# Optimization experiments

Measured on AMD Instinct MI355X. Metric: run time of the kernel, lower is better.

## Reference

```python
import jax, jax.numpy as jnp
import numpy as np
from jax.scipy.special import gammaln, logsumexp

N_SAMPLE, N_GENE, N_TYPE, N_BATCH = 50000, 128, 16, 4


def setup_inputs() -> dict:
    key = jax.random.key(0)
    ks = jax.random.split(key, 7)
    delta = 0.5 * jax.random.normal(ks[0], (N_GENE, N_TYPE), dtype=jnp.float32)
    beta = 0.1 * jax.random.normal(ks[1], (N_BATCH, N_GENE), dtype=jnp.float32)
    # dispersion starts inside the clamp window [1, 100]
    phi = 1.0 + 50.0 * jax.random.uniform(ks[2], (N_GENE,), dtype=jnp.float32)
    # count data (non-negative integers stored as float, as in the torch model)
    expr_mat = jax.random.randint(ks[3], (N_SAMPLE, N_GENE), 0, 20).astype(jnp.float32)
    # design matrix: intercept column + small covariates
    cov = 0.1 * jax.random.uniform(ks[4], (N_SAMPLE, N_BATCH - 1), dtype=jnp.float32)
    cov_mat = jnp.concatenate([jnp.ones((N_SAMPLE, 1), jnp.float32), cov], axis=1)
    # positive size factors around 1
    size_factor = 0.5 + jax.random.uniform(ks[5], (N_SAMPLE,), dtype=jnp.float32)
    marker_onehot = jax.random.randint(ks[6], (N_GENE, N_TYPE), 0, 2).astype(jnp.float32)
    return {"delta": delta, "beta": beta, "phi": phi, "expr_mat": expr_mat,
            "cov_mat": cov_mat, "size_factor": size_factor, "marker_onehot": marker_onehot}


def reference(delta, beta, phi, expr_mat, cov_mat, size_factor, marker_onehot):
    # phi_filter: clamp dispersion to [1, 100]
    phi_f = jnp.clip(phi, 1.0, 100.0)          # [G]
    eta = cov_mat @ beta                        # [S, G] batch effect per gene
    # mu: [S, G, T]
    mu = size_factor[:, None, None] * jnp.exp(eta[:, :, None] + (marker_onehot * delta)[None, :, :])
    phi3 = phi_f[None, :, None]                 # [1, G, 1]
    probs = phi3 / (mu + phi3)                  # NB failure prob param, [S, G, T]
    k = expr_mat[:, :, None]                    # [S, G, 1]
    # nb_logpmf(k, n=phi, p=1-probs) = lgamma(n+k)-lgamma(1+k)-lgamma(n) + k*log(1-probs) + n*log(probs)
    log_pmf = (gammaln(phi3 + k) - gammaln(1.0 + k) - gammaln(phi3)
               + k * jnp.log(1.0 - probs) + phi3 * jnp.log(probs))
    log_probs = log_pmf.sum(axis=1)             # sum over genes -> [S, T]
    log_prob = logsumexp(log_probs, axis=1)     # mixture over cell types -> [S]
    return log_prob.sum()
```

## Files before the change

kernel.cpp:

```cpp
#include <hip/hip_runtime.h>
#include <hip/hip_bf16.h>

#define NG 128
#define NT 16

#define GTAB_OFF 0
#define MD_OFF   1024
#define EMD_OFF  3072
#define LG_OFF   5120
#define TAB_FLOATS 7680
#define LN2 0.6931471805599453f
#define L2E 1.4426950408889634f
#define EXP2F(x) __builtin_amdgcn_exp2f(x)

__global__ void setup_kernel(const float* __restrict__ delta,
                             const float* __restrict__ beta,
                             const float* __restrict__ phi,
                             const float* __restrict__ mo,
                             float* __restrict__ ws,
                             float* __restrict__ out) {
    const int g = threadIdx.x;
    if (g == 0) out[0] = 0.0f;
    if (g >= NG) return;

    const float lnfact[20] = {
        0.0f, 0.0f, 0.69314718f, 1.79175947f, 3.17805383f,
        4.78749174f, 6.57925121f, 8.52516132f, 10.60460286f, 12.80182744f,
        15.10441253f, 17.50230781f, 19.98721446f, 22.55216381f, 25.19122114f,
        27.89927134f, 30.67186007f, 33.50507341f, 36.39544517f, 39.33988415f};

    float ph = fminf(fmaxf(phi[g], 1.0f), 100.0f);
    float plp = ph * __logf(ph);

    ws[GTAB_OFF + g * 8 + 0] = beta[0 * NG + g];
    ws[GTAB_OFF + g * 8 + 1] = beta[1 * NG + g];
    ws[GTAB_OFF + g * 8 + 2] = beta[2 * NG + g];
    ws[GTAB_OFF + g * 8 + 3] = beta[3 * NG + g];
    ws[GTAB_OFF + g * 8 + 4] = ph;
    ws[GTAB_OFF + g * 8 + 5] = 0.0f;
    ws[GTAB_OFF + g * 8 + 6] = 0.0f;
    ws[GTAB_OFF + g * 8 + 7] = 0.0f;

#pragma unroll
    for (int t = 0; t < NT; ++t) {
        float md = mo[g * NT + t] * delta[g * NT + t];
        ws[MD_OFF  + g * 16 + t] = md;
        ws[EMD_OFF + g * 16 + t] = __expf(md);
    }

    float accn = 0.0f;
    ws[LG_OFF + g * 20 + 0] = plp;
#pragma unroll
    for (int k = 1; k < 20; ++k) {
        accn += __logf(ph + (float)(k - 1));
        ws[LG_OFF + g * 20 + k] = accn - lnfact[k] + plp;
    }
}

__global__ __launch_bounds__(512) void nb_main(const float* __restrict__ expr,
                                               const float* __restrict__ cov,
                                               const float* __restrict__ sfv,
                                               const float* __restrict__ ws,
                                               float* __restrict__ out,
                                               int ns) {
    __shared__ float s_tab[TAB_FLOATS];

    const int tid = threadIdx.x;
#pragma unroll
    for (int i = 0; i < 4; ++i) {
        int idx = tid + i * 512;
        if (idx < TAB_FLOATS / 4)
            *(float4*)&s_tab[idx * 4] = *(const float4*)(ws + idx * 4);
    }
    __syncthreads();

    const float* __restrict__ s_gt  = s_tab + GTAB_OFF;
    const float* __restrict__ s_mdp = s_tab + MD_OFF;
    const float* __restrict__ s_emd = s_tab + EMD_OFF;
    const float* __restrict__ s_lg  = s_tab + LG_OFF;

    const int lane = tid & 63;
    const int q = __builtin_amdgcn_readfirstlane(tid >> 6);
    const int s = blockIdx.x * 64 + lane;
    const bool valid = (s < ns);

    float acc[NT];
#pragma unroll
    for (int t = 0; t < NT; ++t) acc[t] = 0.0f;
    float hacc = 0.0f;

    float4 cv = make_float4(0.f, 0.f, 0.f, 0.f);
    float sf = 1.0f;
    if (valid) {
        cv = *reinterpret_cast<const float4*>(cov + (size_t)s * 4);
        sf = sfv[s];
    }
    const float lsf  = __logf(sf);
    const float lsf2 = lsf * L2E;

    const int g0 = q * 16;

    float kb[16];
#pragma unroll
    for (int g4 = 0; g4 < 4; ++g4) {
        float4 kv = make_float4(0.f, 0.f, 0.f, 0.f);
        if (valid)
            kv = *reinterpret_cast<const float4*>(expr + (size_t)s * NG + g0 + g4 * 4);
        kb[g4 * 4 + 0] = kv.x; kb[g4 * 4 + 1] = kv.y;
        kb[g4 * 4 + 2] = kv.z; kb[g4 * 4 + 3] = kv.w;
    }

#pragma unroll 2
    for (int gg = 0; gg < 16; ++gg) {
        const int g = g0 + gg;
        float4 bv = *(const float4*)&s_gt[g * 8];
        float  ph = s_gt[g * 8 + 4];
        float4 ev0 = *(const float4*)&s_emd[g * 16 + 0];
        float4 ev1 = *(const float4*)&s_emd[g * 16 + 4];
        float4 ev2 = *(const float4*)&s_emd[g * 16 + 8];
        float4 ev3 = *(const float4*)&s_emd[g * 16 + 12];
        float4 mv0 = *(const float4*)&s_mdp[g * 16 + 0];
        float4 mv1 = *(const float4*)&s_mdp[g * 16 + 4];
        float4 mv2 = *(const float4*)&s_mdp[g * 16 + 8];
        float4 mv3 = *(const float4*)&s_mdp[g * 16 + 12];

        float e = fmaf(bv.w, cv.w, fmaf(bv.z, cv.z, fmaf(bv.y, cv.y, bv.x * cv.x)));
        float c = EXP2F(fmaf(e, L2E, lsf2));
        float kf = kb[gg];
        float lg = s_lg[g * 20 + (int)kf];
        hacc += fmaf(kf, lsf + e, lg);
        float nkp2 = -(kf + ph) * LN2;

        const float ee[16] = {ev0.x, ev0.y, ev0.z, ev0.w, ev1.x, ev1.y, ev1.z, ev1.w,
                              ev2.x, ev2.y, ev2.z, ev2.w, ev3.x, ev3.y, ev3.z, ev3.w};
        const float mm[16] = {mv0.x, mv0.y, mv0.z, mv0.w, mv1.x, mv1.y, mv1.z, mv1.w,
                              mv2.x, mv2.y, mv2.z, mv2.w, mv3.x, mv3.y, mv3.z, mv3.w};
#pragma unroll
        for (int t = 0; t < NT; ++t) {
            float v = fmaf(c, ee[t], ph);
            acc[t] = fmaf(nkp2, __log2f(v), acc[t]);
        }
#pragma unroll
        for (int t = 0; t < NT; ++t)
            acc[t] = fmaf(kf, mm[t], acc[t]);
    }
#pragma unroll
    for (int t = 0; t < NT; ++t) acc[t] += hacc;

    float (*red)[64][17] = (float (*)[64][17])s_tab;
    __syncthreads();

    if (q >= 4) {
#pragma unroll
        for (int t = 0; t < NT; ++t) red[q - 4][lane][t] = acc[t];
    }
    __syncthreads();
    if (q < 4) {
#pragma unroll
        for (int t = 0; t < NT; ++t) acc[t] += red[q][lane][t];
    }
    __syncthreads();
    if (q == 2 || q == 3) {
#pragma unroll
        for (int t = 0; t < NT; ++t) red[q - 2][lane][t] = acc[t];
    }
    __syncthreads();
    if (q < 2) {
#pragma unroll
        for (int t = 0; t < NT; ++t) acc[t] += red[q][lane][t];
    }
    __syncthreads();
    if (q == 1) {
#pragma unroll
        for (int t = 0; t < NT; ++t) red[0][lane][t] = acc[t];
    }
    __syncthreads();
    if (q == 0) {
        float m = -1e30f;
#pragma unroll
        for (int t = 0; t < NT; ++t) {
            acc[t] += red[0][lane][t];
            m = fmaxf(m, acc[t]);
        }
        float sum = 0.0f;
#pragma unroll
        for (int t = 0; t < NT; ++t) sum += __expf(acc[t] - m);
        float lp = m + __logf(sum);
        if (!valid) lp = 0.0f;
#pragma unroll
        for (int off = 32; off > 0; off >>= 1) lp += __shfl_down(lp, off);
        if (lane == 0) atomicAdd(out, lp);
    }
}

extern "C" void kernel_launch(void* const* d_in, const int* in_sizes, int n_in,
                              void* d_out, int out_size, void* d_ws, size_t ws_size,
                              hipStream_t stream) {
    const float* delta = (const float*)d_in[0];
    const float* beta  = (const float*)d_in[1];
    const float* phi   = (const float*)d_in[2];
    const float* expr  = (const float*)d_in[3];
    const float* cov   = (const float*)d_in[4];
    const float* sf    = (const float*)d_in[5];
    const float* mo    = (const float*)d_in[6];
    float* out = (float*)d_out;
    float* ws  = (float*)d_ws;
    const int ns = in_sizes[5];

    setup_kernel<<<1, 128, 0, stream>>>(delta, beta, phi, mo, ws, out);

    const int tiles = (ns + 63) / 64;
    nb_main<<<tiles, 512, 0, stream>>>(expr, cov, sf, ws, out, ns);
}
```

Measured before the change: 36.55 us.

## Fuse table setup into main kernel and pack per-type tables as bf16

```diff
diff --git a/kernel.cpp b/kernel.cpp
--- a/kernel.cpp
+++ b/kernel.cpp
@@ -3,81 +3,71 @@
 
 #define NG 128
 #define NT 16
-
-#define GTAB_OFF 0
-#define MD_OFF   1024
-#define EMD_OFF  3072
-#define LG_OFF   5120
-#define TAB_FLOATS 7680
 #define LN2 0.6931471805599453f
 #define L2E 1.4426950408889634f
 #define EXP2F(x) __builtin_amdgcn_exp2f(x)
 
-__global__ void setup_kernel(const float* __restrict__ delta,
-                             const float* __restrict__ beta,
-                             const float* __restrict__ phi,
-                             const float* __restrict__ mo,
-                             float* __restrict__ ws,
-                             float* __restrict__ out) {
-    const int g = threadIdx.x;
-    if (g == 0) out[0] = 0.0f;
-    if (g >= NG) return;
-
-    const float lnfact[20] = {
-        0.0f, 0.0f, 0.69314718f, 1.79175947f, 3.17805383f,
-        4.78749174f, 6.57925121f, 8.52516132f, 10.60460286f, 12.80182744f,
-        15.10441253f, 17.50230781f, 19.98721446f, 22.55216381f, 25.19122114f,
-        27.89927134f, 30.67186007f, 33.50507341f, 36.39544517f, 39.33988415f};
-
-    float ph = fminf(fmaxf(phi[g], 1.0f), 100.0f);
-    float plp = ph * __logf(ph);
-
-    ws[GTAB_OFF + g * 8 + 0] = beta[0 * NG + g];
-    ws[GTAB_OFF + g * 8 + 1] = beta[1 * NG + g];
-    ws[GTAB_OFF + g * 8 + 2] = beta[2 * NG + g];
-    ws[GTAB_OFF + g * 8 + 3] = beta[3 * NG + g];
-    ws[GTAB_OFF + g * 8 + 4] = ph;
-    ws[GTAB_OFF + g * 8 + 5] = 0.0f;
-    ws[GTAB_OFF + g * 8 + 6] = 0.0f;
-    ws[GTAB_OFF + g * 8 + 7] = 0.0f;
-
-#pragma unroll
-    for (int t = 0; t < NT; ++t) {
-        float md = mo[g * NT + t] * delta[g * NT + t];
-        ws[MD_OFF  + g * 16 + t] = md;
-        ws[EMD_OFF + g * 16 + t] = __expf(md);
-    }
-
-    float accn = 0.0f;
-    ws[LG_OFF + g * 20 + 0] = plp;
-#pragma unroll
-    for (int k = 1; k < 20; ++k) {
-        accn += __logf(ph + (float)(k - 1));
-        ws[LG_OFF + g * 20 + k] = accn - lnfact[k] + plp;
-    }
-}
-
-__global__ __launch_bounds__(512) void nb_main(const float* __restrict__ expr,
-                                               const float* __restrict__ cov,
-                                               const float* __restrict__ sfv,
-                                               const float* __restrict__ ws,
-                                               float* __restrict__ out,
-                                               int ns) {
-    __shared__ float s_tab[TAB_FLOATS];
+__global__ void zero_out(float* __restrict__ out) {
+    if (threadIdx.x == 0) out[0] = 0.0f;
+}
+
+__device__ __forceinline__ unsigned short f2bf(float x) {
+    unsigned b = __float_as_uint(x);
+    unsigned r = (b + 0x7FFFu + ((b >> 16) & 1u)) >> 16;
+    return (unsigned short)r;
+}
+__device__ __forceinline__ float bf_lo(unsigned u) { return __uint_as_float(u << 16); }
+__device__ __forceinline__ float bf_hi(unsigned u) { return __uint_as_float(u & 0xFFFF0000u); }
+
+__global__ __launch_bounds__(512, 4) void nb_main(const float* __restrict__ delta,
+                                                  const float* __restrict__ beta,
+                                                  const float* __restrict__ phi,
+                                                  const float* __restrict__ mo,
+                                                  const float* __restrict__ expr,
+                                                  const float* __restrict__ cov,
+                                                  const float* __restrict__ sfv,
+                                                  float* __restrict__ out,
+                                                  int ns) {
+    __shared__ __align__(16) unsigned char s_mem[22528];
+    float*          s_gt  = (float*)s_mem;
+    unsigned short* s_e16 = (unsigned short*)(s_mem + 4096);
+    float*          s_lg  = (float*)(s_mem + 12288);
 
     const int tid = threadIdx.x;
-#pragma unroll
-    for (int i = 0; i < 4; ++i) {
-        int idx = tid + i * 512;
-        if (idx < TAB_FLOATS / 4)
-            *(float4*)&s_tab[idx * 4] = *(const float4*)(ws + idx * 4);
-    }
-    __syncthreads();
-
-    const float* __restrict__ s_gt  = s_tab + GTAB_OFF;
-    const float* __restrict__ s_mdp = s_tab + MD_OFF;
-    const float* __restrict__ s_emd = s_tab + EMD_OFF;
-    const float* __restrict__ s_lg  = s_tab + LG_OFF;
+
+    if (tid < NG) {
+        const int g = tid;
+        const float lnfact[20] = {
+            0.0f, 0.0f, 0.69314718f, 1.79175947f, 3.17805383f,
+            4.78749174f, 6.57925121f, 8.52516132f, 10.60460286f, 12.80182744f,
+            15.10441253f, 17.50230781f, 19.98721446f, 22.55216381f, 25.19122114f,
+            27.89927134f, 30.67186007f, 33.50507341f, 36.39544517f, 39.33988415f};
+
+        float ph = fminf(fmaxf(phi[g], 1.0f), 100.0f);
+        float plp = ph * __logf(ph);
+
+        s_gt[g * 8 + 0] = beta[0 * NG + g];
+        s_gt[g * 8 + 1] = beta[1 * NG + g];
+        s_gt[g * 8 + 2] = beta[2 * NG + g];
+        s_gt[g * 8 + 3] = beta[3 * NG + g];
+        s_gt[g * 8 + 4] = ph;
+
+#pragma unroll
+        for (int t = 0; t < NT; ++t) {
+            float md = mo[g * NT + t] * delta[g * NT + t];
+            s_e16[g * 32 + t]      = f2bf(__expf(md));
+            s_e16[g * 32 + 16 + t] = f2bf(md);
+        }
+
+        float accn = 0.0f;
+        s_lg[g * 20 + 0] = plp;
+#pragma unroll
+        for (int k = 1; k < 20; ++k) {
+            accn += __logf(ph + (float)(k - 1));
+            s_lg[g * 20 + k] = accn - lnfact[k] + plp;
+        }
+    }
+    __syncthreads();
 
     const int lane = tid & 63;
     const int q = __builtin_amdgcn_readfirstlane(tid >> 6);
@@ -113,16 +103,13 @@
 #pragma unroll 2
     for (int gg = 0; gg < 16; ++gg) {
         const int g = g0 + gg;
+        const uint4* eu = (const uint4*)&s_e16[g * 32];
+        uint4 E0 = eu[0];
+        uint4 E1 = eu[1];
+        uint4 M0 = eu[2];
+        uint4 M1 = eu[3];
         float4 bv = *(const float4*)&s_gt[g * 8];
         float  ph = s_gt[g * 8 + 4];
-        float4 ev0 = *(const float4*)&s_emd[g * 16 + 0];
-        float4 ev1 = *(const float4*)&s_emd[g * 16 + 4];
-        float4 ev2 = *(const float4*)&s_emd[g * 16 + 8];
-        float4 ev3 = *(const float4*)&s_emd[g * 16 + 12];
-        float4 mv0 = *(const float4*)&s_mdp[g * 16 + 0];
-        float4 mv1 = *(const float4*)&s_mdp[g * 16 + 4];
-        float4 mv2 = *(const float4*)&s_mdp[g * 16 + 8];
-        float4 mv3 = *(const float4*)&s_mdp[g * 16 + 12];
 
         float e = fmaf(bv.w, cv.w, fmaf(bv.z, cv.z, fmaf(bv.y, cv.y, bv.x * cv.x)));
         float c = EXP2F(fmaf(e, L2E, lsf2));
@@ -131,23 +118,26 @@
         hacc += fmaf(kf, lsf + e, lg);
         float nkp2 = -(kf + ph) * LN2;
 
-        const float ee[16] = {ev0.x, ev0.y, ev0.z, ev0.w, ev1.x, ev1.y, ev1.z, ev1.w,
-                              ev2.x, ev2.y, ev2.z, ev2.w, ev3.x, ev3.y, ev3.z, ev3.w};
-        const float mm[16] = {mv0.x, mv0.y, mv0.z, mv0.w, mv1.x, mv1.y, mv1.z, mv1.w,
-                              mv2.x, mv2.y, mv2.z, mv2.w, mv3.x, mv3.y, mv3.z, mv3.w};
+        float ee[16], mm[16];
+        ee[0] = bf_lo(E0.x); ee[1] = bf_hi(E0.x); ee[2] = bf_lo(E0.y); ee[3] = bf_hi(E0.y);
+        ee[4] = bf_lo(E0.z); ee[5] = bf_hi(E0.z); ee[6] = bf_lo(E0.w); ee[7] = bf_hi(E0.w);
+        ee[8] = bf_lo(E1.x); ee[9] = bf_hi(E1.x); ee[10] = bf_lo(E1.y); ee[11] = bf_hi(E1.y);
+        ee[12] = bf_lo(E1.z); ee[13] = bf_hi(E1.z); ee[14] = bf_lo(E1.w); ee[15] = bf_hi(E1.w);
+        mm[0] = bf_lo(M0.x); mm[1] = bf_hi(M0.x); mm[2] = bf_lo(M0.y); mm[3] = bf_hi(M0.y);
+        mm[4] = bf_lo(M0.z); mm[5] = bf_hi(M0.z); mm[6] = bf_lo(M0.w); mm[7] = bf_hi(M0.w);
+        mm[8] = bf_lo(M1.x); mm[9] = bf_hi(M1.x); mm[10] = bf_lo(M1.y); mm[11] = bf_hi(M1.y);
+        mm[12] = bf_lo(M1.z); mm[13] = bf_hi(M1.z); mm[14] = bf_lo(M1.w); mm[15] = bf_hi(M1.w);
+
 #pragma unroll
         for (int t = 0; t < NT; ++t) {
             float v = fmaf(c, ee[t], ph);
-            acc[t] = fmaf(nkp2, __log2f(v), acc[t]);
-        }
-#pragma unroll
-        for (int t = 0; t < NT; ++t)
-            acc[t] = fmaf(kf, mm[t], acc[t]);
+            acc[t] = fmaf(nkp2, __log2f(v), fmaf(kf, mm[t], acc[t]));
+        }
     }
 #pragma unroll
     for (int t = 0; t < NT; ++t) acc[t] += hacc;
 
-    float (*red)[64][17] = (float (*)[64][17])s_tab;
+    float (*red)[64][17] = (float (*)[64][17])s_mem;
     __syncthreads();
 
     if (q >= 4) {
@@ -204,11 +194,9 @@
     const float* sf    = (const float*)d_in[5];
     const float* mo    = (const float*)d_in[6];
     float* out = (float*)d_out;
-    float* ws  = (float*)d_ws;
     const int ns = in_sizes[5];
 
-    setup_kernel<<<1, 128, 0, stream>>>(delta, beta, phi, mo, ws, out);
-
+    zero_out<<<1, 64, 0, stream>>>(out);
     const int tiles = (ns + 63) / 64;
-    nb_main<<<tiles, 512, 0, stream>>>(expr, cov, sf, ws, out, ns);
-}
+    nb_main<<<tiles, 512, 0, stream>>>(delta, beta, phi, mo, expr, cov, sf, out, ns);
+}
```

Result: slower. 41.77 us (+14.3%).

## Transpose shared tables and swap loop order to iterate types outer, genes inner

Applied to the files above, without the earlier changes.

```diff
diff --git a/kernel.cpp b/kernel.cpp
--- a/kernel.cpp
+++ b/kernel.cpp
@@ -4,9 +4,10 @@
 #define NG 128
 #define NT 16
 
-#define GTAB_OFF 0
-#define MD_OFF   1024
-#define EMD_OFF  3072
+#define BT_OFF   0
+#define PH_OFF   512
+#define EMD_OFF  1024
+#define MD_OFF   3072
 #define LG_OFF   5120
 #define TAB_FLOATS 7680
 #define LN2 0.6931471805599453f
@@ -32,20 +33,16 @@
     float ph = fminf(fmaxf(phi[g], 1.0f), 100.0f);
     float plp = ph * __logf(ph);
 
-    ws[GTAB_OFF + g * 8 + 0] = beta[0 * NG + g];
-    ws[GTAB_OFF + g * 8 + 1] = beta[1 * NG + g];
-    ws[GTAB_OFF + g * 8 + 2] = beta[2 * NG + g];
-    ws[GTAB_OFF + g * 8 + 3] = beta[3 * NG + g];
-    ws[GTAB_OFF + g * 8 + 4] = ph;
-    ws[GTAB_OFF + g * 8 + 5] = 0.0f;
-    ws[GTAB_OFF + g * 8 + 6] = 0.0f;
-    ws[GTAB_OFF + g * 8 + 7] = 0.0f;
+#pragma unroll
+    for (int j = 0; j < 4; ++j)
+        ws[BT_OFF + j * NG + g] = beta[j * NG + g];
+    ws[PH_OFF + g] = ph;
 
 #pragma unroll
     for (int t = 0; t < NT; ++t) {
         float md = mo[g * NT + t] * delta[g * NT + t];
-        ws[MD_OFF  + g * 16 + t] = md;
-        ws[EMD_OFF + g * 16 + t] = __expf(md);
+        ws[EMD_OFF + t * NG + g] = __expf(md);
+        ws[MD_OFF  + t * NG + g] = md;
     }
 
     float accn = 0.0f;
@@ -74,20 +71,16 @@
     }
     __syncthreads();
 
-    const float* __restrict__ s_gt  = s_tab + GTAB_OFF;
-    const float* __restrict__ s_mdp = s_tab + MD_OFF;
+    const float* __restrict__ s_bT  = s_tab + BT_OFF;
+    const float* __restrict__ s_ph  = s_tab + PH_OFF;
     const float* __restrict__ s_emd = s_tab + EMD_OFF;
+    const float* __restrict__ s_md  = s_tab + MD_OFF;
     const float* __restrict__ s_lg  = s_tab + LG_OFF;
 
     const int lane = tid & 63;
     const int q = __builtin_amdgcn_readfirstlane(tid >> 6);
     const int s = blockIdx.x * 64 + lane;
     const bool valid = (s < ns);
-
-    float acc[NT];
-#pragma unroll
-    for (int t = 0; t < NT; ++t) acc[t] = 0.0f;
-    float hacc = 0.0f;
 
     float4 cv = make_float4(0.f, 0.f, 0.f, 0.f);
     float sf = 1.0f;
@@ -100,52 +93,69 @@
 
     const int g0 = q * 16;
 
-    float kb[16];
-#pragma unroll
-    for (int g4 = 0; g4 < 4; ++g4) {
-        float4 kv = make_float4(0.f, 0.f, 0.f, 0.f);
-        if (valid)
-            kv = *reinterpret_cast<const float4*>(expr + (size_t)s * NG + g0 + g4 * 4);
-        kb[g4 * 4 + 0] = kv.x; kb[g4 * 4 + 1] = kv.y;
-        kb[g4 * 4 + 2] = kv.z; kb[g4 * 4 + 3] = kv.w;
-    }
-
-#pragma unroll 2
-    for (int gg = 0; gg < 16; ++gg) {
-        const int g = g0 + gg;
-        float4 bv = *(const float4*)&s_gt[g * 8];
-        float  ph = s_gt[g * 8 + 4];
-        float4 ev0 = *(const float4*)&s_emd[g * 16 + 0];
-        float4 ev1 = *(const float4*)&s_emd[g * 16 + 4];
-        float4 ev2 = *(const float4*)&s_emd[g * 16 + 8];
-        float4 ev3 = *(const float4*)&s_emd[g * 16 + 12];
-        float4 mv0 = *(const float4*)&s_mdp[g * 16 + 0];
-        float4 mv1 = *(const float4*)&s_mdp[g * 16 + 4];
-        float4 mv2 = *(const float4*)&s_mdp[g * 16 + 8];
-        float4 mv3 = *(const float4*)&s_mdp[g * 16 + 12];
-
-        float e = fmaf(bv.w, cv.w, fmaf(bv.z, cv.z, fmaf(bv.y, cv.y, bv.x * cv.x)));
-        float c = EXP2F(fmaf(e, L2E, lsf2));
-        float kf = kb[gg];
-        float lg = s_lg[g * 20 + (int)kf];
-        hacc += fmaf(kf, lsf + e, lg);
-        float nkp2 = -(kf + ph) * LN2;
-
-        const float ee[16] = {ev0.x, ev0.y, ev0.z, ev0.w, ev1.x, ev1.y, ev1.z, ev1.w,
-                              ev2.x, ev2.y, ev2.z, ev2.w, ev3.x, ev3.y, ev3.z, ev3.w};
-        const float mm[16] = {mv0.x, mv0.y, mv0.z, mv0.w, mv1.x, mv1.y, mv1.z, mv1.w,
-                              mv2.x, mv2.y, mv2.z, mv2.w, mv3.x, mv3.y, mv3.z, mv3.w};
-#pragma unroll
-        for (int t = 0; t < NT; ++t) {
-            float v = fmaf(c, ee[t], ph);
-            acc[t] = fmaf(nkp2, __log2f(v), acc[t]);
-        }
-#pragma unroll
-        for (int t = 0; t < NT; ++t)
-            acc[t] = fmaf(kf, mm[t], acc[t]);
-    }
-#pragma unroll
-    for (int t = 0; t < NT; ++t) acc[t] += hacc;
+    float kf[16], cc[16], nkp[16], phv[16];
+    float hacc = 0.0f;
+    {
+#pragma unroll
+        for (int g4 = 0; g4 < 4; ++g4) {
+            float4 kv = make_float4(0.f, 0.f, 0.f, 0.f);
+            if (valid)
+                kv = *reinterpret_cast<const float4*>(expr + (size_t)s * NG + g0 + g4 * 4);
+            kf[g4 * 4 + 0] = kv.x; kf[g4 * 4 + 1] = kv.y;
+            kf[g4 * 4 + 2] = kv.z; kf[g4 * 4 + 3] = kv.w;
+        }
+        float ev[16];
+#pragma unroll
+        for (int g4 = 0; g4 < 4; ++g4) {
+            float4 b0 = *(const float4*)&s_bT[0 * NG + g0 + g4 * 4];
+            float4 b1 = *(const float4*)&s_bT[1 * NG + g0 + g4 * 4];
+            float4 b2 = *(const float4*)&s_bT[2 * NG + g0 + g4 * 4];
+            float4 b3 = *(const float4*)&s_bT[3 * NG + g0 + g4 * 4];
+            ev[g4 * 4 + 0] = fmaf(b3.x, cv.w, fmaf(b2.x, cv.z, fmaf(b1.x, cv.y, b0.x * cv.x)));
+            ev[g4 * 4 + 1] = fmaf(b3.y, cv.w, fmaf(b2.y, cv.z, fmaf(b1.y, cv.y, b0.y * cv.x)));
+            ev[g4 * 4 + 2] = fmaf(b3.z, cv.w, fmaf(b2.z, cv.z, fmaf(b1.z, cv.y, b0.z * cv.x)));
+            ev[g4 * 4 + 3] = fmaf(b3.w, cv.w, fmaf(b2.w, cv.z, fmaf(b1.w, cv.y, b0.w * cv.x)));
+        }
+#pragma unroll
+        for (int g4 = 0; g4 < 4; ++g4) {
+            float4 p = *(const float4*)&s_ph[g0 + g4 * 4];
+            phv[g4 * 4 + 0] = p.x; phv[g4 * 4 + 1] = p.y;
+            phv[g4 * 4 + 2] = p.z; phv[g4 * 4 + 3] = p.w;
+        }
+#pragma unroll
+        for (int gg = 0; gg < 16; ++gg) {
+            cc[gg] = EXP2F(fmaf(ev[gg], L2E, lsf2));
+            float lg = s_lg[(g0 + gg) * 20 + (int)kf[gg]];
+            hacc += fmaf(kf[gg], lsf + ev[gg], lg);
+            nkp[gg] = -(kf[gg] + phv[gg]) * LN2;
+        }
+    }
+
+    float acc[NT];
+#pragma unroll 4
+    for (int t = 0; t < NT; ++t) {
+        float4 e0 = *(const float4*)&s_emd[t * NG + g0 + 0];
+        float4 e1 = *(const float4*)&s_emd[t * NG + g0 + 4];
+        float4 e2 = *(const float4*)&s_emd[t * NG + g0 + 8];
+        float4 e3 = *(const float4*)&s_emd[t * NG + g0 + 12];
+        float4 m0 = *(const float4*)&s_md[t * NG + g0 + 0];
+        float4 m1 = *(const float4*)&s_md[t * NG + g0 + 4];
+        float4 m2 = *(const float4*)&s_md[t * NG + g0 + 8];
+        float4 m3 = *(const float4*)&s_md[t * NG + g0 + 12];
+        const float ee[16] = {e0.x, e0.y, e0.z, e0.w, e1.x, e1.y, e1.z, e1.w,
+                              e2.x, e2.y, e2.z, e2.w, e3.x, e3.y, e3.z, e3.w};
+        const float mm[16] = {m0.x, m0.y, m0.z, m0.w, m1.x, m1.y, m1.z, m1.w,
+                              m2.x, m2.y, m2.z, m2.w, m3.x, m3.y, m3.z, m3.w};
+        float p0 = 0.0f, p1 = 0.0f;
+#pragma unroll
+        for (int gg = 0; gg < 16; gg += 2) {
+            float v0 = fmaf(cc[gg], ee[gg], phv[gg]);
+            p0 = fmaf(nkp[gg], __log2f(v0), fmaf(kf[gg], mm[gg], p0));
+            float v1 = fmaf(cc[gg + 1], ee[gg + 1], phv[gg + 1]);
+            p1 = fmaf(nkp[gg + 1], __log2f(v1), fmaf(kf[gg + 1], mm[gg + 1], p1));
+        }
+        acc[t] = p0 + p1 + hacc;
+    }
 
     float (*red)[64][17] = (float (*)[64][17])s_tab;
     __syncthreads();
```

New measurement: 37.44 us. 2.4% more time.
